# Optimization experiments

Hardware: AMD Instinct MI355X
Metric: run time of the kernel (lower is better)

The kernel has to match this reference:

```python
import jax, jax.numpy as jnp
import numpy as np


def setup_inputs() -> dict:
    key = jax.random.key(0)
    k1, k2, k3, k4 = jax.random.split(key, 4)
    N, E, DIN, DOUT = 16384, 8192, 128, 128
    x = jax.random.normal(k1, (N, DIN), dtype=jnp.float32)
    # sparse binary incidence matrix, avg node degree ~ E * 0.005 ~ 41
    H = (jax.random.uniform(k2, (N, E)) < 0.005).astype(jnp.float32)
    W = jax.random.normal(k3, (DOUT, DIN), dtype=jnp.float32) * (1.0 / np.sqrt(DIN))
    b = jax.random.normal(k4, (DOUT,), dtype=jnp.float32) * 0.01
    return {"x": x, "H": H, "W": W, "b": b}


def reference(x, H, W, b):
    # Degree vectors. Original builds dense diag matrices; off-diagonal zeros
    # raised to negative powers become inf and are zeroed by nan_to_num, so the
    # math reduces to elementwise inverse powers of the degree vectors with
    # non-finite entries mapped to 0.
    deg_node = jnp.sum(H, axis=1)                    # [N]
    deg_edge = jnp.sum(H, axis=0)                    # [E]
    dvih = jnp.where(deg_node > 0, deg_node ** -0.5, 0.0)   # D_v^{-1/2}
    dei = jnp.where(deg_edge > 0, 1.0 / deg_edge, 0.0)      # D_e^{-1}
    # D_v^{-1/2} H D_e^{-1} H^T D_v^{-1/2} x, as broadcasted row scalings
    y = dvih[:, None] * x                            # [N, DIN]
    y = H.T @ y                                      # [E, DIN]
    y = dei[:, None] * y                             # [E, DIN]
    y = H @ y                                        # [N, DIN]
    y = dvih[:, None] * y                            # [N, DIN]
    return y @ W.T + b                               # [N, DOUT]
```

## Files before the change

kernel.cpp:

```cpp
#include <hip/hip_runtime.h>
#include <hip/hip_bf16.h>

#define NN 16384
#define EE 8192
#define DD 128
#define CSR_STRIDE 128
#define CSC_STRIDE 192

__device__ __forceinline__ unsigned short f2bf(float f) {
    union { float f; unsigned u; } c; c.f = f;
    unsigned u = c.u + (0x7FFFu + ((c.u >> 16) & 1u));
    return (unsigned short)(u >> 16);
}
__device__ __forceinline__ float bf2f(unsigned short h) {
    union { unsigned u; float f; } c; c.u = ((unsigned)h) << 16;
    return c.f;
}


__global__ __launch_bounds__(256) void g_gemm(
    const float* __restrict__ x,
    const float* __restrict__ W,
    ushort4* __restrict__ xwb,
    int* __restrict__ edge_cnt)
{
    const int t = threadIdx.x;
    {
        int tid = blockIdx.x * 256 + t;
        if (tid < EE) edge_cnt[tid] = 0;
    }

    __shared__ float sA[32 * 132];
    __shared__ float sW[64 * 132];
    const int m0 = blockIdx.x * 32;

#pragma unroll
    for (int r = 0; r < 16; ++r) {
        int i = t + 256 * r;
        int row = i >> 7, col = i & 127;
        sA[row * 132 + col] = x[(size_t)(m0 + row) * DD + col];
    }

    const int jg = t & 15;
    const int mg = t >> 4;
    const int m2 = mg * 2;
    const int j4 = jg * 4;

    for (int h = 0; h < 2; ++h) {
        __syncthreads();
#pragma unroll
        for (int r = 0; r < 32; ++r) {
            int i = t + 256 * r;
            int row = i >> 7, col = i & 127;
            sW[row * 132 + col] = W[(size_t)(h * 64 + row) * DD + col];
        }
        __syncthreads();

        float acc0[4] = {0.f, 0.f, 0.f, 0.f};
        float acc1[4] = {0.f, 0.f, 0.f, 0.f};
#pragma unroll 4
        for (int k = 0; k < 128; k += 4) {
            float4 a0 = *(const float4*)&sA[m2 * 132 + k];
            float4 a1 = *(const float4*)&sA[(m2 + 1) * 132 + k];
#pragma unroll
            for (int jj = 0; jj < 4; ++jj) {
                float4 w = *(const float4*)&sW[(j4 + jj) * 132 + k];
                acc0[jj] += a0.x*w.x + a0.y*w.y + a0.z*w.z + a0.w*w.w;
                acc1[jj] += a1.x*w.x + a1.y*w.y + a1.z*w.z + a1.w*w.w;
            }
        }
        ushort4 p0, p1;
        p0.x = f2bf(acc0[0]); p0.y = f2bf(acc0[1]); p0.z = f2bf(acc0[2]); p0.w = f2bf(acc0[3]);
        p1.x = f2bf(acc1[0]); p1.y = f2bf(acc1[1]); p1.z = f2bf(acc1[2]); p1.w = f2bf(acc1[3]);
        xwb[(size_t)(m0 + m2)     * 32 + h * 16 + jg] = p0;
        xwb[(size_t)(m0 + m2 + 1) * 32 + h * 16 + jg] = p1;
    }
}

__global__ __launch_bounds__(256) void k1_parse(
    const float* __restrict__ H,
    float* __restrict__ dvih,
    int* __restrict__ csr_cnt,
    int* __restrict__ csr_idx,
    int* __restrict__ edge_cnt,
    int* __restrict__ csc_idx)
{
    const int n = blockIdx.x;
    const int t = threadIdx.x;
    __shared__ int s_cnt;
    __shared__ int s_list[CSR_STRIDE];
    if (t == 0) s_cnt = 0;
    __syncthreads();

    const float4* row = (const float4*)(H + (size_t)n * EE);
#pragma unroll
    for (int j = 0; j < 8; ++j) {
        int idx = t + 256 * j;
        float4 v = row[idx];
        int base = idx * 4;
        if (v.x != 0.0f) { int p = atomicAdd(&s_cnt, 1); if (p < CSR_STRIDE) s_list[p] = base + 0; }
        if (v.y != 0.0f) { int p = atomicAdd(&s_cnt, 1); if (p < CSR_STRIDE) s_list[p] = base + 1; }
        if (v.z != 0.0f) { int p = atomicAdd(&s_cnt, 1); if (p < CSR_STRIDE) s_list[p] = base + 2; }
        if (v.w != 0.0f) { int p = atomicAdd(&s_cnt, 1); if (p < CSR_STRIDE) s_list[p] = base + 3; }
    }
    __syncthreads();

    int cnt = s_cnt; if (cnt > CSR_STRIDE) cnt = CSR_STRIDE;
    if (t < cnt) {
        int e = s_list[t];
        csr_idx[(size_t)n * CSR_STRIDE + t] = e;
        int pos = atomicAdd(&edge_cnt[e], 1);
        if (pos < CSC_STRIDE) csc_idx[(size_t)e * CSC_STRIDE + pos] = n;
    }
    if (t == 0) {
        csr_cnt[n] = cnt;
        dvih[n] = (cnt > 0) ? (1.0f / sqrtf((float)cnt)) : 0.0f;
    }
}

__global__ __launch_bounds__(256) void k2_edge_gather(
    const ushort4* __restrict__ xwb,
    const float* __restrict__ dvih,
    const int* __restrict__ edge_cnt,
    const int* __restrict__ csc_idx,
    ushort4* __restrict__ y2b)
{
    const int t    = threadIdx.x;
    const int sub  = t >> 7;
    const int tt   = t & 127;
    const int grp  = tt >> 5;
    const int lane = tt & 31;
    const int e    = blockIdx.x * 2 + sub;

    __shared__ int    s_lst[2][CSC_STRIDE];
    __shared__ float  s_dv[2][CSC_STRIDE];
    __shared__ float4 s_red[2][3][32];

    int cnt = edge_cnt[e];
    int ccnt = cnt > CSC_STRIDE ? CSC_STRIDE : cnt;
    for (int i = tt; i < ccnt; i += 128) {
        int n = csc_idx[(size_t)e * CSC_STRIDE + i];
        s_lst[sub][i] = n;
        s_dv[sub][i]  = dvih[n];
    }
    __syncthreads();

    float ax = 0.f, ay = 0.f, az = 0.f, aw = 0.f;
    int i = grp;
    for (; i + 16 <= ccnt; i += 16) {
        ushort4 v0 = xwb[(size_t)s_lst[sub][i     ] * 32 + lane];
        ushort4 v1 = xwb[(size_t)s_lst[sub][i +  4] * 32 + lane];
        ushort4 v2 = xwb[(size_t)s_lst[sub][i +  8] * 32 + lane];
        ushort4 v3 = xwb[(size_t)s_lst[sub][i + 12] * 32 + lane];
        float f0 = s_dv[sub][i], f1 = s_dv[sub][i + 4];
        float f2 = s_dv[sub][i + 8], f3 = s_dv[sub][i + 12];
        ax += f0*bf2f(v0.x) + f1*bf2f(v1.x) + f2*bf2f(v2.x) + f3*bf2f(v3.x);
        ay += f0*bf2f(v0.y) + f1*bf2f(v1.y) + f2*bf2f(v2.y) + f3*bf2f(v3.y);
        az += f0*bf2f(v0.z) + f1*bf2f(v1.z) + f2*bf2f(v2.z) + f3*bf2f(v3.z);
        aw += f0*bf2f(v0.w) + f1*bf2f(v1.w) + f2*bf2f(v2.w) + f3*bf2f(v3.w);
    }
    for (; i < ccnt; i += 4) {
        ushort4 v = xwb[(size_t)s_lst[sub][i] * 32 + lane];
        float f = s_dv[sub][i];
        ax += f*bf2f(v.x); ay += f*bf2f(v.y); az += f*bf2f(v.z); aw += f*bf2f(v.w);
    }

    if (grp) { s_red[sub][grp - 1][lane] = make_float4(ax, ay, az, aw); }
    __syncthreads();
    if (grp == 0) {
        float4 r0 = s_red[sub][0][lane];
        float4 r1 = s_red[sub][1][lane];
        float4 r2 = s_red[sub][2][lane];
        float dei = (cnt > 0) ? (1.0f / (float)cnt) : 0.0f;
        ushort4 o;
        o.x = f2bf((ax + r0.x + r1.x + r2.x) * dei);
        o.y = f2bf((ay + r0.y + r1.y + r2.y) * dei);
        o.z = f2bf((az + r0.z + r1.z + r2.z) * dei);
        o.w = f2bf((aw + r0.w + r1.w + r2.w) * dei);
        y2b[(size_t)e * 32 + lane] = o;
    }
}

__global__ __launch_bounds__(256) void k3_node_gather(
    const ushort4* __restrict__ y2b,
    const float* __restrict__ dvih,
    const int* __restrict__ csr_cnt,
    const int* __restrict__ csr_idx,
    const float* __restrict__ b,
    float* __restrict__ out)
{
    const int t    = threadIdx.x;
    const int sub  = t >> 7;
    const int tt   = t & 127;
    const int grp  = tt >> 5;
    const int lane = tt & 31;
    const int n    = blockIdx.x * 2 + sub;

    __shared__ int    s_lst[2][CSR_STRIDE];
    __shared__ float4 s_red[2][3][32];

    int cnt = csr_cnt[n];
    if (tt < cnt) s_lst[sub][tt] = csr_idx[(size_t)n * CSR_STRIDE + tt];
    __syncthreads();

    float ax = 0.f, ay = 0.f, az = 0.f, aw = 0.f;
    int i = grp;
    for (; i + 16 <= cnt; i += 16) {
        ushort4 v0 = y2b[(size_t)s_lst[sub][i     ] * 32 + lane];
        ushort4 v1 = y2b[(size_t)s_lst[sub][i +  4] * 32 + lane];
        ushort4 v2 = y2b[(size_t)s_lst[sub][i +  8] * 32 + lane];
        ushort4 v3 = y2b[(size_t)s_lst[sub][i + 12] * 32 + lane];
        ax += bf2f(v0.x) + bf2f(v1.x) + bf2f(v2.x) + bf2f(v3.x);
        ay += bf2f(v0.y) + bf2f(v1.y) + bf2f(v2.y) + bf2f(v3.y);
        az += bf2f(v0.z) + bf2f(v1.z) + bf2f(v2.z) + bf2f(v3.z);
        aw += bf2f(v0.w) + bf2f(v1.w) + bf2f(v2.w) + bf2f(v3.w);
    }
    for (; i < cnt; i += 4) {
        ushort4 v = y2b[(size_t)s_lst[sub][i] * 32 + lane];
        ax += bf2f(v.x); ay += bf2f(v.y); az += bf2f(v.z); aw += bf2f(v.w);
    }

    if (grp) { s_red[sub][grp - 1][lane] = make_float4(ax, ay, az, aw); }
    __syncthreads();
    if (grp == 0) {
        float4 r0 = s_red[sub][0][lane];
        float4 r1 = s_red[sub][1][lane];
        float4 r2 = s_red[sub][2][lane];
        float dv = dvih[n];
        float4 bb = ((const float4*)b)[lane];
        float4 o = make_float4((ax + r0.x + r1.x + r2.x) * dv + bb.x,
                               (ay + r0.y + r1.y + r2.y) * dv + bb.y,
                               (az + r0.z + r1.z + r2.z) * dv + bb.z,
                               (aw + r0.w + r1.w + r2.w) * dv + bb.w);
        ((float4*)out)[(size_t)n * 32 + lane] = o;
    }
}

extern "C" void kernel_launch(void* const* d_in, const int* in_sizes, int n_in,
                              void* d_out, int out_size, void* d_ws, size_t ws_size,
                              hipStream_t stream) {
    const float* x = (const float*)d_in[0];
    const float* H = (const float*)d_in[1];
    const float* W = (const float*)d_in[2];
    const float* b = (const float*)d_in[3];
    float* out = (float*)d_out;

    char* ws = (char*)d_ws;
    float*   dvih    = (float*)  (ws + 0);
    int*     csr_cnt = (int*)    (ws + 65536);
    int*     edge_cnt= (int*)    (ws + 131072);
    int*     csr_idx = (int*)    (ws + 163840);
    int*     csc_idx = (int*)    (ws + 8552448);
    ushort4* xwb     = (ushort4*)(ws + 14843904);
    ushort4* y2b     = (ushort4*)(ws + 19038208);

    g_gemm<<<NN / 32, 256, 0, stream>>>(x, W, xwb, edge_cnt);
    k1_parse<<<NN, 256, 0, stream>>>(H, dvih, csr_cnt, csr_idx, edge_cnt, csc_idx);
    k2_edge_gather<<<EE / 2, 256, 0, stream>>>(xwb, dvih, edge_cnt, csc_idx, y2b);
    k3_node_gather<<<NN / 2, 256, 0, stream>>>(y2b, dvih, csr_cnt, csr_idx, b, out);
}
```

Measured before the change: 755.5 us.

## Use one wavefront per row in gathers, shuffle reduce, nontemporal H loads

Result: faster. 729.9 us (-3.4%).

```diff
diff --git a/kernel.cpp b/kernel.cpp
--- a/kernel.cpp
+++ b/kernel.cpp
@@ -7,6 +7,8 @@
 #define CSR_STRIDE 128
 #define CSC_STRIDE 192
 
+typedef float vfloat4 __attribute__((ext_vector_type(4)));
+
 __device__ __forceinline__ unsigned short f2bf(float f) {
     union { float f; unsigned u; } c; c.f = f;
     unsigned u = c.u + (0x7FFFu + ((c.u >> 16) & 1u));
@@ -35,10 +37,11 @@
     const int m0 = blockIdx.x * 32;
 
 #pragma unroll
-    for (int r = 0; r < 16; ++r) {
+    for (int r = 0; r < 4; ++r) {
         int i = t + 256 * r;
-        int row = i >> 7, col = i & 127;
-        sA[row * 132 + col] = x[(size_t)(m0 + row) * DD + col];
+        int row = i >> 5, c4 = (i & 31) << 2;
+        *(float4*)&sA[row * 132 + c4] =
+            *(const float4*)&x[(size_t)(m0 + row) * DD + c4];
     }
 
     const int jg = t & 15;
@@ -49,10 +52,11 @@
     for (int h = 0; h < 2; ++h) {
         __syncthreads();
 #pragma unroll
-        for (int r = 0; r < 32; ++r) {
+        for (int r = 0; r < 8; ++r) {
             int i = t + 256 * r;
-            int row = i >> 7, col = i & 127;
-            sW[row * 132 + col] = W[(size_t)(h * 64 + row) * DD + col];
+            int row = i >> 5, c4 = (i & 31) << 2;
+            *(float4*)&sW[row * 132 + c4] =
+                *(const float4*)&W[(size_t)(h * 64 + row) * DD + c4];
         }
         __syncthreads();
 
@@ -92,16 +96,16 @@
     if (t == 0) s_cnt = 0;
     __syncthreads();
 
-    const float4* row = (const float4*)(H + (size_t)n * EE);
+    const vfloat4* row = (const vfloat4*)(H + (size_t)n * EE);
 #pragma unroll
     for (int j = 0; j < 8; ++j) {
         int idx = t + 256 * j;
-        float4 v = row[idx];
+        vfloat4 v = __builtin_nontemporal_load(row + idx);
         int base = idx * 4;
-        if (v.x != 0.0f) { int p = atomicAdd(&s_cnt, 1); if (p < CSR_STRIDE) s_list[p] = base + 0; }
-        if (v.y != 0.0f) { int p = atomicAdd(&s_cnt, 1); if (p < CSR_STRIDE) s_list[p] = base + 1; }
-        if (v.z != 0.0f) { int p = atomicAdd(&s_cnt, 1); if (p < CSR_STRIDE) s_list[p] = base + 2; }
-        if (v.w != 0.0f) { int p = atomicAdd(&s_cnt, 1); if (p < CSR_STRIDE) s_list[p] = base + 3; }
+        if (v[0] != 0.0f) { int p = atomicAdd(&s_cnt, 1); if (p < CSR_STRIDE) s_list[p] = base + 0; }
+        if (v[1] != 0.0f) { int p = atomicAdd(&s_cnt, 1); if (p < CSR_STRIDE) s_list[p] = base + 1; }
+        if (v[2] != 0.0f) { int p = atomicAdd(&s_cnt, 1); if (p < CSR_STRIDE) s_list[p] = base + 2; }
+        if (v[3] != 0.0f) { int p = atomicAdd(&s_cnt, 1); if (p < CSR_STRIDE) s_list[p] = base + 3; }
     }
     __syncthreads();
 
@@ -126,58 +130,67 @@
     ushort4* __restrict__ y2b)
 {
     const int t    = threadIdx.x;
-    const int sub  = t >> 7;
-    const int tt   = t & 127;
-    const int grp  = tt >> 5;
-    const int lane = tt & 31;
-    const int e    = blockIdx.x * 2 + sub;
-
-    __shared__ int    s_lst[2][CSC_STRIDE];
-    __shared__ float  s_dv[2][CSC_STRIDE];
-    __shared__ float4 s_red[2][3][32];
+    const int w    = t >> 6;
+    const int lane = t & 63;
+    const int grp  = lane >> 5;
+    const int fl   = lane & 31;
+    const int e    = blockIdx.x * 4 + w;
+
+    __shared__ int    s_lst[4][CSC_STRIDE];
+    __shared__ float  s_dv[4][CSC_STRIDE];
 
     int cnt = edge_cnt[e];
     int ccnt = cnt > CSC_STRIDE ? CSC_STRIDE : cnt;
-    for (int i = tt; i < ccnt; i += 128) {
+    for (int i = lane; i < ccnt; i += 64) {
         int n = csc_idx[(size_t)e * CSC_STRIDE + i];
-        s_lst[sub][i] = n;
-        s_dv[sub][i]  = dvih[n];
+        s_lst[w][i] = n;
+        s_dv[w][i]  = dvih[n];
     }
     __syncthreads();
 
     float ax = 0.f, ay = 0.f, az = 0.f, aw = 0.f;
     int i = grp;
-    for (; i + 16 <= ccnt; i += 16) {
-        ushort4 v0 = xwb[(size_t)s_lst[sub][i     ] * 32 + lane];
-        ushort4 v1 = xwb[(size_t)s_lst[sub][i +  4] * 32 + lane];
-        ushort4 v2 = xwb[(size_t)s_lst[sub][i +  8] * 32 + lane];
-        ushort4 v3 = xwb[(size_t)s_lst[sub][i + 12] * 32 + lane];
-        float f0 = s_dv[sub][i], f1 = s_dv[sub][i + 4];
-        float f2 = s_dv[sub][i + 8], f3 = s_dv[sub][i + 12];
-        ax += f0*bf2f(v0.x) + f1*bf2f(v1.x) + f2*bf2f(v2.x) + f3*bf2f(v3.x);
-        ay += f0*bf2f(v0.y) + f1*bf2f(v1.y) + f2*bf2f(v2.y) + f3*bf2f(v3.y);
-        az += f0*bf2f(v0.z) + f1*bf2f(v1.z) + f2*bf2f(v2.z) + f3*bf2f(v3.z);
-        aw += f0*bf2f(v0.w) + f1*bf2f(v1.w) + f2*bf2f(v2.w) + f3*bf2f(v3.w);
-    }
-    for (; i < ccnt; i += 4) {
-        ushort4 v = xwb[(size_t)s_lst[sub][i] * 32 + lane];
-        float f = s_dv[sub][i];
+    for (; i + 14 < ccnt; i += 16) {
+        ushort4 v0 = xwb[(size_t)s_lst[w][i     ] * 32 + fl];
+        ushort4 v1 = xwb[(size_t)s_lst[w][i +  2] * 32 + fl];
+        ushort4 v2 = xwb[(size_t)s_lst[w][i +  4] * 32 + fl];
+        ushort4 v3 = xwb[(size_t)s_lst[w][i +  6] * 32 + fl];
+        ushort4 v4 = xwb[(size_t)s_lst[w][i +  8] * 32 + fl];
+        ushort4 v5 = xwb[(size_t)s_lst[w][i + 10] * 32 + fl];
+        ushort4 v6 = xwb[(size_t)s_lst[w][i + 12] * 32 + fl];
+        ushort4 v7 = xwb[(size_t)s_lst[w][i + 14] * 32 + fl];
+        float f0 = s_dv[w][i],      f1 = s_dv[w][i +  2];
+        float f2 = s_dv[w][i +  4], f3 = s_dv[w][i +  6];
+        float f4 = s_dv[w][i +  8], f5 = s_dv[w][i + 10];
+        float f6 = s_dv[w][i + 12], f7 = s_dv[w][i + 14];
+        ax += f0*bf2f(v0.x) + f1*bf2f(v1.x) + f2*bf2f(v2.x) + f3*bf2f(v3.x)
+            + f4*bf2f(v4.x) + f5*bf2f(v5.x) + f6*bf2f(v6.x) + f7*bf2f(v7.x);
+        ay += f0*bf2f(v0.y) + f1*bf2f(v1.y) + f2*bf2f(v2.y) + f3*bf2f(v3.y)
+            + f4*bf2f(v4.y) + f5*bf2f(v5.y) + f6*bf2f(v6.y) + f7*bf2f(v7.y);
+        az += f0*bf2f(v0.z) + f1*bf2f(v1.z) + f2*bf2f(v2.z) + f3*bf2f(v3.z)
+            + f4*bf2f(v4.z) + f5*bf2f(v5.z) + f6*bf2f(v6.z) + f7*bf2f(v7.z);
+        aw += f0*bf2f(v0.w) + f1*bf2f(v1.w) + f2*bf2f(v2.w) + f3*bf2f(v3.w)
+            + f4*bf2f(v4.w) + f5*bf2f(v5.w) + f6*bf2f(v6.w) + f7*bf2f(v7.w);
+    }
+    for (; i < ccnt; i += 2) {
+        ushort4 v = xwb[(size_t)s_lst[w][i] * 32 + fl];
+        float f = s_dv[w][i];
         ax += f*bf2f(v.x); ay += f*bf2f(v.y); az += f*bf2f(v.z); aw += f*bf2f(v.w);
     }
 
-    if (grp) { s_red[sub][grp - 1][lane] = make_float4(ax, ay, az, aw); }
-    __syncthreads();
+    ax += __shfl_xor(ax, 32);
+    ay += __shfl_xor(ay, 32);
+    az += __shfl_xor(az, 32);
+    aw += __shfl_xor(aw, 32);
+
     if (grp == 0) {
-        float4 r0 = s_red[sub][0][lane];
-        float4 r1 = s_red[sub][1][lane];
-        float4 r2 = s_red[sub][2][lane];
         float dei = (cnt > 0) ? (1.0f / (float)cnt) : 0.0f;
         ushort4 o;
-        o.x = f2bf((ax + r0.x + r1.x + r2.x) * dei);
-        o.y = f2bf((ay + r0.y + r1.y + r2.y) * dei);
-        o.z = f2bf((az + r0.z + r1.z + r2.z) * dei);
-        o.w = f2bf((aw + r0.w + r1.w + r2.w) * dei);
-        y2b[(size_t)e * 32 + lane] = o;
+        o.x = f2bf(ax * dei);
+        o.y = f2bf(ay * dei);
+        o.z = f2bf(az * dei);
+        o.w = f2bf(aw * dei);
+        y2b[(size_t)e * 32 + fl] = o;
     }
 }
 
@@ -190,49 +203,49 @@
     float* __restrict__ out)
 {
     const int t    = threadIdx.x;
-    const int sub  = t >> 7;
-    const int tt   = t & 127;
-    const int grp  = tt >> 5;
-    const int lane = tt & 31;
-    const int n    = blockIdx.x * 2 + sub;
-
-    __shared__ int    s_lst[2][CSR_STRIDE];
-    __shared__ float4 s_red[2][3][32];
+    const int w    = t >> 6;
+    const int lane = t & 63;
+    const int grp  = lane >> 5;
+    const int fl   = lane & 31;
+    const int n    = blockIdx.x * 4 + w;
+
+    __shared__ int s_lst[4][CSR_STRIDE];
 
     int cnt = csr_cnt[n];
-    if (tt < cnt) s_lst[sub][tt] = csr_idx[(size_t)n * CSR_STRIDE + tt];
+    for (int i = lane; i < cnt; i += 64)
+        s_lst[w][i] = csr_idx[(size_t)n * CSR_STRIDE + i];
     __syncthreads();
 
     float ax = 0.f, ay = 0.f, az = 0.f, aw = 0.f;
     int i = grp;
-    for (; i + 16 <= cnt; i += 16) {
-        ushort4 v0 = y2b[(size_t)s_lst[sub][i     ] * 32 + lane];
-        ushort4 v1 = y2b[(size_t)s_lst[sub][i +  4] * 32 + lane];
-        ushort4 v2 = y2b[(size_t)s_lst[sub][i +  8] * 32 + lane];
-        ushort4 v3 = y2b[(size_t)s_lst[sub][i + 12] * 32 + lane];
+    for (; i + 6 < cnt; i += 8) {
+        ushort4 v0 = y2b[(size_t)s_lst[w][i    ] * 32 + fl];
+        ushort4 v1 = y2b[(size_t)s_lst[w][i + 2] * 32 + fl];
+        ushort4 v2 = y2b[(size_t)s_lst[w][i + 4] * 32 + fl];
+        ushort4 v3 = y2b[(size_t)s_lst[w][i + 6] * 32 + fl];
         ax += bf2f(v0.x) + bf2f(v1.x) + bf2f(v2.x) + bf2f(v3.x);
         ay += bf2f(v0.y) + bf2f(v1.y) + bf2f(v2.y) + bf2f(v3.y);
         az += bf2f(v0.z) + bf2f(v1.z) + bf2f(v2.z) + bf2f(v3.z);
         aw += bf2f(v0.w) + bf2f(v1.w) + bf2f(v2.w) + bf2f(v3.w);
     }
-    for (; i < cnt; i += 4) {
-        ushort4 v = y2b[(size_t)s_lst[sub][i] * 32 + lane];
+    for (; i < cnt; i += 2) {
+        ushort4 v = y2b[(size_t)s_lst[w][i] * 32 + fl];
         ax += bf2f(v.x); ay += bf2f(v.y); az += bf2f(v.z); aw += bf2f(v.w);
     }
 
-    if (grp) { s_red[sub][grp - 1][lane] = make_float4(ax, ay, az, aw); }
-    __syncthreads();
+    ax += __shfl_xor(ax, 32);
+    ay += __shfl_xor(ay, 32);
+    az += __shfl_xor(az, 32);
+    aw += __shfl_xor(aw, 32);
+
     if (grp == 0) {
-        float4 r0 = s_red[sub][0][lane];
-        float4 r1 = s_red[sub][1][lane];
-        float4 r2 = s_red[sub][2][lane];
         float dv = dvih[n];
-        float4 bb = ((const float4*)b)[lane];
-        float4 o = make_float4((ax + r0.x + r1.x + r2.x) * dv + bb.x,
-                               (ay + r0.y + r1.y + r2.y) * dv + bb.y,
-                               (az + r0.z + r1.z + r2.z) * dv + bb.z,
-                               (aw + r0.w + r1.w + r2.w) * dv + bb.w);
-        ((float4*)out)[(size_t)n * 32 + lane] = o;
+        float4 bb = ((const float4*)b)[fl];
+        float4 o = make_float4(ax * dv + bb.x,
+                               ay * dv + bb.y,
+                               az * dv + bb.z,
+                               aw * dv + bb.w);
+        ((float4*)out)[(size_t)n * 32 + fl] = o;
     }
 }
 
@@ -256,6 +269,6 @@
 
     g_gemm<<<NN / 32, 256, 0, stream>>>(x, W, xwb, edge_cnt);
     k1_parse<<<NN, 256, 0, stream>>>(H, dvih, csr_cnt, csr_idx, edge_cnt, csc_idx);
-    k2_edge_gather<<<EE / 2, 256, 0, stream>>>(xwb, dvih, edge_cnt, csc_idx, y2b);
-    k3_node_gather<<<NN / 2, 256, 0, stream>>>(y2b, dvih, csr_cnt, csr_idx, b, out);
-}
+    k2_edge_gather<<<EE / 4, 256, 0, stream>>>(xwb, dvih, edge_cnt, csc_idx, y2b);
+    k3_node_gather<<<NN / 4, 256, 0, stream>>>(y2b, dvih, csr_cnt, csr_idx, b, out);
+}
```
